# Kernel optimization log

Hardware: AMD Instinct MI355X
Metric: run time of the kernel (lower is better)

The kernel has to match this reference:

```python
import jax, jax.numpy as jnp
import numpy as np

SIGMA = 0.5          # init kwarg sigma
PATCH = 5            # init kwarg patch_size
TILE = 32            # init kwarg patch_distance (tile side)
H_PARAM = (PATCH // 2) ** 0.5  # self.h = sqrt(patch_size//2)


def _nlm(tiles, sigma, p, Hp):
    # tiles: [b, c, h, w] -- faithful jax port of nlm()
    b, c, h, w = tiles.shape
    pad = p // 2
    padded = jnp.pad(tiles, ((0, 0), (0, 0), (pad, pad), (pad, pad)), mode='edge')  # replicate pad
    # unfold: all p*p shifted views -> [b, c, p*p, h, w] (channel-major then patch index,
    # matching torch unfold + unflatten(1, (c, p*p)))
    pats = jnp.stack([padded[:, :, i:i + h, j:j + w]
                      for i in range(p) for j in range(p)], axis=2)
    center = p * p // 2
    keep = np.array([k for k in range(p * p) if k != center])
    N = h * w
    d = c * (p * p - 1)
    yN = pats[:, :, keep].reshape(b, d, N).transpose(0, 2, 1)  # [b, N, d]
    # pairwise euclidean distance (cdist)
    sq = jnp.sum(yN * yN, axis=-1)  # [b, N]
    d2 = sq[:, :, None] + sq[:, None, :] - 2.0 * jnp.einsum('bnd,bmd->bnm', yN, yN)
    dist = jnp.sqrt(jnp.maximum(d2, 0.0))  # [b, N, N]
    density = jnp.exp(-dist / (2.0 * Hp ** 2 * sigma ** 2))
    # diag set to +inf in dist -> density diag = 0
    density = density * (1.0 - jnp.eye(N, dtype=density.dtype))
    weight = density / jnp.sum(density, axis=-1, keepdims=True)  # [b, N, N]
    y = tiles.reshape(b, c, N)  # [b, c, N]
    mmse = jnp.einsum('bnm,bcm->bcn', weight, y)  # weighted sum of pixel values
    return mmse.reshape(b, c, h, w)


def reference(image):
    # Tile image into non-overlapping TILE x TILE tiles, run nlm batched, fold back.
    b, c, h, w = image.shape
    T = TILE
    nh, nw = h // T, w // T
    tiles = image.reshape(b, c, nh, T, nw, T).transpose(0, 2, 4, 1, 3, 5)
    tiles = tiles.reshape(b * nh * nw, c, T, T)
    out = _nlm(tiles, SIGMA, PATCH, H_PARAM)
    out = out.reshape(b, nh, nw, c, T, T).transpose(0, 3, 1, 4, 2, 5)
    return out.reshape(b, c, h, w)


def setup_inputs() -> dict:
    key = jax.random.key(0)
    image = jax.random.uniform(key, (1, 3, 320, 320), dtype=jnp.float32)
    return {"image": image}
```

## Files before the change

kernel.cpp:

```cpp
#include <hip/hip_runtime.h>
#include <math.h>

#define TS   32
#define PT   36
#define NPIX 1024
#define DF   72
#define KP   96
#define IMH  320
#define IMW  320
#define NTW  10
#define NTILE 100

#define F_UNITS_PER_TILE 12288
#define FHI_BYTES (NTILE * F_UNITS_PER_TILE * 16)
#define SQ_OFF    (2 * FHI_BYTES)

#define K2LOG2E 2.0813689810056077f

typedef __attribute__((ext_vector_type(8))) short bf16x8;
typedef __attribute__((ext_vector_type(8))) unsigned short u16x8;
typedef __attribute__((ext_vector_type(4))) float f32x4;

__global__ __launch_bounds__(256)
void nlm_feat_kernel(const float* __restrict__ img,
                     u16x8* __restrict__ Fhi, float* __restrict__ Sq)
{
    __shared__ float Ploc[3][6][36];
    __shared__ int   ofsl[KP];
    const int tid  = threadIdx.x;
    const int part = blockIdx.x;
    const int tile = blockIdx.y;
    const int by   = (tile / NTW) * TS;
    const int bx   = (tile % NTW) * TS;
    const float* Pf = &Ploc[0][0][0];

    for (int idx = tid; idx < 3 * 6 * 36; idx += 256) {
        int c   = idx / 216;
        int rem = idx - c * 216;
        int yl  = rem / 36;
        int x   = rem - yl * 36;
        int y   = 2 * part + yl;
        int iy  = min(max(y - 2, 0), TS - 1);
        int ix  = min(max(x - 2, 0), TS - 1);
        Ploc[c][yl][x] = img[(c * IMH + by + iy) * IMW + bx + ix];
    }
    if (tid < KP) {
        int k = tid, v = 0;
        if (k < DF) {
            int c = k / 24, o = k - c * 24;
            int kk = o + (o >= 12);
            int i = kk / 5, j = kk - (kk / 5) * 5;
            v = c * 216 + i * 36 + j;
        }
        ofsl[k] = v;
    }
    __syncthreads();

    if (tid < 64) {
        int m  = part * 64 + tid;
        int my = m >> 5, mx = m & 31;
        int ly0 = my - 2 * part;
        float s = 0.f;
        #pragma unroll
        for (int k = 0; k < 25; ++k) {
            if (k == 12) continue;
            int i = k / 5, j = k - (k / 5) * 5;
            float v0 = Ploc[0][ly0 + i][mx + j];
            float v1 = Ploc[1][ly0 + i][mx + j];
            float v2 = Ploc[2][ly0 + i][mx + j];
            s = fmaf(v0, v0, s); s = fmaf(v1, v1, s); s = fmaf(v2, v2, s);
        }
        Sq[tile * NPIX + m] = s;
    }

    #pragma unroll
    for (int q = 0; q < 3; ++q) {
        int u    = part * 768 + q * 256 + tid;
        int row  = u & 15;
        int c4   = (u >> 4) & 3;
        int rks  = u >> 6;
        int ks   = rks - (rks / 3) * 3;
        int rt   = rks / 3;
        int r    = rt * 16 + row;
        int lbase = ((r >> 5) - 2 * part) * 36 + (r & 31);
        u16x8 h;
        #pragma unroll
        for (int j = 0; j < 8; ++j) {
            int k = ks * 32 + c4 * 8 + j;
            unsigned short hs = 0;
            if (k < DF) {
                float f = Pf[lbase + ofsl[k]];
                unsigned int uu = __float_as_uint(f);
                hs = (unsigned short)((uu + 0x7fffu + ((uu >> 16) & 1u)) >> 16);
            }
            h[j] = hs;
        }
        Fhi[tile * F_UNITS_PER_TILE + u] = h;
    }
}

__global__ __launch_bounds__(256)
__attribute__((amdgpu_waves_per_eu(2, 3)))
void nlm_gemm_kernel(const float* __restrict__ img,
                     const bf16x8* __restrict__ Fhi,
                     const float* __restrict__ Sq, float* __restrict__ out)
{
    __shared__ float red[4][32][4];
    const int tid  = threadIdx.x;
    const int lane = tid & 63;
    const int wv   = tid >> 6;
    const int tile = blockIdx.y;
    const int by   = (tile / NTW) * TS;
    const int bx   = (tile % NTW) * TS;
    const int rtA  = blockIdx.x * 2;
    const int quad = lane >> 4;
    const int col  = lane & 15;

    const bf16x8* FHt = Fhi + tile * F_UNITS_PER_TILE;
    const float*  Sqt = Sq + tile * NPIX;

    bf16x8 aH[2][3];
    #pragma unroll
    for (int t = 0; t < 2; ++t)
        #pragma unroll
        for (int ks = 0; ks < 3; ++ks)
            aH[t][ks] = FHt[((rtA + t) * 3 + ks) * 64 + lane];
    asm volatile(""
        : "+v"(aH[0][0]), "+v"(aH[0][1]), "+v"(aH[0][2]),
          "+v"(aH[1][0]), "+v"(aH[1][1]), "+v"(aH[1][2]));

    float sqnK[2][4];
    #pragma unroll
    for (int t = 0; t < 2; ++t)
        #pragma unroll
        for (int i = 0; i < 4; ++i)
            sqnK[t][i] = Sqt[(rtA + t) * 16 + quad * 4 + i] * K2LOG2E;

    float rowsum[2][4] = {};
    float oacc[2][4][3] = {};

    #pragma unroll 2
    for (int it = 0; it < 16; ++it) {
        const int mt = wv * 16 + it;
        bf16x8 bH[3];
        #pragma unroll
        for (int ks = 0; ks < 3; ++ks)
            bH[ks] = FHt[(mt * 3 + ks) * 64 + lane];
        const int m  = mt * 16 + col;
        float smK = Sqt[m] * K2LOG2E;
        int my = m >> 5, mx = m & 31;
        float y0 = img[(0 * IMH + by + my) * IMW + bx + mx];
        float y1 = img[(1 * IMH + by + my) * IMW + bx + mx];
        float y2 = img[(2 * IMH + by + my) * IMW + bx + mx];

        f32x4 C0 = {0.f, 0.f, 0.f, 0.f};
        f32x4 C1 = {0.f, 0.f, 0.f, 0.f};
        #pragma unroll
        for (int ks = 0; ks < 3; ++ks) {
            C0 = __builtin_amdgcn_mfma_f32_16x16x32_bf16(aH[0][ks], bH[ks], C0, 0, 0, 0);
            C1 = __builtin_amdgcn_mfma_f32_16x16x32_bf16(aH[1][ks], bH[ks], C1, 0, 0, 0);
        }
        #pragma unroll
        for (int t = 0; t < 2; ++t) {
            f32x4 C = t ? C1 : C0;
            int nb = (rtA + t) * 16 + quad * 4;
            #pragma unroll
            for (int i = 0; i < 4; ++i) {
                float s2   = fmaxf(fmaf(-2.0f * K2LOG2E, C[i], sqnK[t][i] + smK), 0.f);
                float dens = __builtin_amdgcn_exp2f(-__builtin_amdgcn_sqrtf(s2));
                if (m == nb + i) dens = 0.f;
                rowsum[t][i] += dens;
                oacc[t][i][0] = fmaf(dens, y0, oacc[t][i][0]);
                oacc[t][i][1] = fmaf(dens, y1, oacc[t][i][1]);
                oacc[t][i][2] = fmaf(dens, y2, oacc[t][i][2]);
            }
        }
    }

    #pragma unroll
    for (int mask = 1; mask < 16; mask <<= 1)
        #pragma unroll
        for (int t = 0; t < 2; ++t)
            #pragma unroll
            for (int i = 0; i < 4; ++i) {
                rowsum[t][i]  += __shfl_xor(rowsum[t][i],  mask, 64);
                oacc[t][i][0] += __shfl_xor(oacc[t][i][0], mask, 64);
                oacc[t][i][1] += __shfl_xor(oacc[t][i][1], mask, 64);
                oacc[t][i][2] += __shfl_xor(oacc[t][i][2], mask, 64);
            }

    if (col == 0) {
        #pragma unroll
        for (int t = 0; t < 2; ++t)
            #pragma unroll
            for (int i = 0; i < 4; ++i) {
                int lr = t * 16 + quad * 4 + i;
                red[wv][lr][0] = rowsum[t][i];
                red[wv][lr][1] = oacc[t][i][0];
                red[wv][lr][2] = oacc[t][i][1];
                red[wv][lr][3] = oacc[t][i][2];
            }
    }
    __syncthreads();

    if (tid < 32) {
        float s = 0.f, o0 = 0.f, o1 = 0.f, o2 = 0.f;
        #pragma unroll
        for (int w = 0; w < 4; ++w) {
            s  += red[w][tid][0];
            o0 += red[w][tid][1];
            o1 += red[w][tid][2];
            o2 += red[w][tid][3];
        }
        int n = rtA * 16 + tid;
        float inv = 1.f / s;
        int gy = by + (n >> 5), gx = bx + (n & 31);
        out[(0 * IMH + gy) * IMW + gx] = o0 * inv;
        out[(1 * IMH + gy) * IMW + gx] = o1 * inv;
        out[(2 * IMH + gy) * IMW + gx] = o2 * inv;
    }
}

extern "C" void kernel_launch(void* const* d_in, const int* in_sizes, int n_in,
                              void* d_out, int out_size, void* d_ws, size_t ws_size,
                              hipStream_t stream) {
    const float* img = (const float*)d_in[0];
    float* out = (float*)d_out;
    char* ws = (char*)d_ws;
    u16x8* Fhi = (u16x8*)ws;
    float* Sq  = (float*)(ws + SQ_OFF);

    dim3 fgrid(16, NTILE);
    nlm_feat_kernel<<<fgrid, 256, 0, stream>>>(img, Fhi, Sq);
    dim3 grid(32, NTILE);
    nlm_gemm_kernel<<<grid, 256, 0, stream>>>(img, (const bf16x8*)Fhi, Sq, out);
}
```

Baseline: 113.8 us.

## Compute weighted pixel sums and row sums with fp16 MFMA instead of VALU FMAs

The second product (density times pixel values, plus the row sum via a constant-one channel) now runs on 16x16x16 fp16 MFMA instead of per-lane FMAs followed by cross-lane shuffle reductions. Pixel values are staged in LDS as hi/lo fp16 pairs to keep precision, and the density is packed to fp16 with round-toward-zero conversion. The operand roles are swapped so the density tile lands directly in the A-operand layout, and the K2LOG2E scaling of the squared norms moves into the feature kernel. This removes the many FMAs and shuffle reductions per element but adds LDS staging, a barrier, and fp16 rounding error on the weights.

```diff
diff --git a/kernel.cpp b/kernel.cpp
--- a/kernel.cpp
+++ b/kernel.cpp
@@ -20,6 +20,8 @@
 typedef __attribute__((ext_vector_type(8))) short bf16x8;
 typedef __attribute__((ext_vector_type(8))) unsigned short u16x8;
 typedef __attribute__((ext_vector_type(4))) float f32x4;
+typedef __attribute__((ext_vector_type(4))) __fp16 f16x4;
+typedef __attribute__((ext_vector_type(2))) __fp16 f16x2;
 
 __global__ __launch_bounds__(256)
 void nlm_feat_kernel(const float* __restrict__ img,
@@ -70,7 +72,7 @@
             float v2 = Ploc[2][ly0 + i][mx + j];
             s = fmaf(v0, v0, s); s = fmaf(v1, v1, s); s = fmaf(v2, v2, s);
         }
-        Sq[tile * NPIX + m] = s;
+        Sq[tile * NPIX + m] = s * K2LOG2E;
     }
 
     #pragma unroll
@@ -103,9 +105,12 @@
 __attribute__((amdgpu_waves_per_eu(2, 3)))
 void nlm_gemm_kernel(const float* __restrict__ img,
                      const bf16x8* __restrict__ Fhi,
-                     const float* __restrict__ Sq, float* __restrict__ out)
+                     const float* __restrict__ SqK, float* __restrict__ out)
 {
-    __shared__ float red[4][32][4];
+    __shared__ __fp16 Yhi[4][1032];
+    __shared__ __fp16 Ylo[4][1032];
+    __shared__ float red[4][2][16][4];
+
     const int tid  = threadIdx.x;
     const int lane = tid & 63;
     const int wv   = tid >> 6;
@@ -115,109 +120,107 @@
     const int rtA  = blockIdx.x * 2;
     const int quad = lane >> 4;
     const int col  = lane & 15;
+    const int ycol = col & 3;
 
     const bf16x8* FHt = Fhi + tile * F_UNITS_PER_TILE;
-    const float*  Sqt = Sq + tile * NPIX;
-
-    bf16x8 aH[2][3];
+    const float*  Sqt = SqK + tile * NPIX;
+
+    for (int idx = tid; idx < 4096; idx += 256) {
+        int c = idx >> 10, m = idx & 1023;
+        float v = 1.0f;
+        if (c < 3) v = img[(c * IMH + by + (m >> 5)) * IMW + bx + (m & 31)];
+        __fp16 h = (__fp16)v;
+        Yhi[c][m] = h;
+        Ylo[c][m] = (__fp16)(v - (float)h);
+    }
+
+    bf16x8 bN[2][3];
     #pragma unroll
     for (int t = 0; t < 2; ++t)
         #pragma unroll
         for (int ks = 0; ks < 3; ++ks)
-            aH[t][ks] = FHt[((rtA + t) * 3 + ks) * 64 + lane];
+            bN[t][ks] = FHt[((rtA + t) * 3 + ks) * 64 + lane];
     asm volatile(""
-        : "+v"(aH[0][0]), "+v"(aH[0][1]), "+v"(aH[0][2]),
-          "+v"(aH[1][0]), "+v"(aH[1][1]), "+v"(aH[1][2]));
-
-    float sqnK[2][4];
+        : "+v"(bN[0][0]), "+v"(bN[0][1]), "+v"(bN[0][2]),
+          "+v"(bN[1][0]), "+v"(bN[1][1]), "+v"(bN[1][2]));
+
+    float snK[2];
     #pragma unroll
     for (int t = 0; t < 2; ++t)
-        #pragma unroll
-        for (int i = 0; i < 4; ++i)
-            sqnK[t][i] = Sqt[(rtA + t) * 16 + quad * 4 + i] * K2LOG2E;
-
-    float rowsum[2][4] = {};
-    float oacc[2][4][3] = {};
+        snK[t] = Sqt[(rtA + t) * 16 + col];
+
+    f32x4 Dpv0 = {0.f, 0.f, 0.f, 0.f};
+    f32x4 Dpv1 = {0.f, 0.f, 0.f, 0.f};
+
+    __syncthreads();
 
     #pragma unroll 2
     for (int it = 0; it < 16; ++it) {
         const int mt = wv * 16 + it;
-        bf16x8 bH[3];
+        bf16x8 aF[3];
         #pragma unroll
         for (int ks = 0; ks < 3; ++ks)
-            bH[ks] = FHt[(mt * 3 + ks) * 64 + lane];
-        const int m  = mt * 16 + col;
-        float smK = Sqt[m] * K2LOG2E;
-        int my = m >> 5, mx = m & 31;
-        float y0 = img[(0 * IMH + by + my) * IMW + bx + mx];
-        float y1 = img[(1 * IMH + by + my) * IMW + bx + mx];
-        float y2 = img[(2 * IMH + by + my) * IMW + bx + mx];
+            aF[ks] = FHt[(mt * 3 + ks) * 64 + lane];
+        const f32x4 sqm = *(const f32x4*)&Sqt[mt * 16 + quad * 4];
+        const int yb = mt * 16 + quad * 4;
+        const f16x4 bhi = *(const f16x4*)&Yhi[ycol][yb];
+        const f16x4 blo = *(const f16x4*)&Ylo[ycol][yb];
 
         f32x4 C0 = {0.f, 0.f, 0.f, 0.f};
         f32x4 C1 = {0.f, 0.f, 0.f, 0.f};
         #pragma unroll
         for (int ks = 0; ks < 3; ++ks) {
-            C0 = __builtin_amdgcn_mfma_f32_16x16x32_bf16(aH[0][ks], bH[ks], C0, 0, 0, 0);
-            C1 = __builtin_amdgcn_mfma_f32_16x16x32_bf16(aH[1][ks], bH[ks], C1, 0, 0, 0);
-        }
+            C0 = __builtin_amdgcn_mfma_f32_16x16x32_bf16(aF[ks], bN[0][ks], C0, 0, 0, 0);
+            C1 = __builtin_amdgcn_mfma_f32_16x16x32_bf16(aF[ks], bN[1][ks], C1, 0, 0, 0);
+        }
+
         #pragma unroll
         for (int t = 0; t < 2; ++t) {
             f32x4 C = t ? C1 : C0;
-            int nb = (rtA + t) * 16 + quad * 4;
+            float d[4];
             #pragma unroll
             for (int i = 0; i < 4; ++i) {
-                float s2   = fmaxf(fmaf(-2.0f * K2LOG2E, C[i], sqnK[t][i] + smK), 0.f);
-                float dens = __builtin_amdgcn_exp2f(-__builtin_amdgcn_sqrtf(s2));
-                if (m == nb + i) dens = 0.f;
-                rowsum[t][i] += dens;
-                oacc[t][i][0] = fmaf(dens, y0, oacc[t][i][0]);
-                oacc[t][i][1] = fmaf(dens, y1, oacc[t][i][1]);
-                oacc[t][i][2] = fmaf(dens, y2, oacc[t][i][2]);
-            }
-        }
-    }
-
-    #pragma unroll
-    for (int mask = 1; mask < 16; mask <<= 1)
-        #pragma unroll
-        for (int t = 0; t < 2; ++t)
-            #pragma unroll
-            for (int i = 0; i < 4; ++i) {
-                rowsum[t][i]  += __shfl_xor(rowsum[t][i],  mask, 64);
-                oacc[t][i][0] += __shfl_xor(oacc[t][i][0], mask, 64);
-                oacc[t][i][1] += __shfl_xor(oacc[t][i][1], mask, 64);
-                oacc[t][i][2] += __shfl_xor(oacc[t][i][2], mask, 64);
-            }
-
-    if (col == 0) {
-        #pragma unroll
-        for (int t = 0; t < 2; ++t)
-            #pragma unroll
-            for (int i = 0; i < 4; ++i) {
-                int lr = t * 16 + quad * 4 + i;
-                red[wv][lr][0] = rowsum[t][i];
-                red[wv][lr][1] = oacc[t][i][0];
-                red[wv][lr][2] = oacc[t][i][1];
-                red[wv][lr][3] = oacc[t][i][2];
-            }
+                float s2 = fmaxf(fmaf(-2.0f * K2LOG2E, C[i], sqm[i] + snK[t]), 0.f);
+                d[i] = __builtin_amdgcn_exp2f(-__builtin_amdgcn_sqrtf(s2));
+            }
+            if (mt == rtA + t) {
+                #pragma unroll
+                for (int i = 0; i < 4; ++i)
+                    if (quad * 4 + i == col) d[i] = 0.f;
+            }
+            f16x2 p0 = __builtin_amdgcn_cvt_pkrtz(d[0], d[1]);
+            f16x2 p1 = __builtin_amdgcn_cvt_pkrtz(d[2], d[3]);
+            f16x4 wp = __builtin_shufflevector(p0, p1, 0, 1, 2, 3);
+            if (t == 0) {
+                Dpv0 = __builtin_amdgcn_mfma_f32_16x16x16f16(wp, bhi, Dpv0, 0, 0, 0);
+                Dpv0 = __builtin_amdgcn_mfma_f32_16x16x16f16(wp, blo, Dpv0, 0, 0, 0);
+            } else {
+                Dpv1 = __builtin_amdgcn_mfma_f32_16x16x16f16(wp, bhi, Dpv1, 0, 0, 0);
+                Dpv1 = __builtin_amdgcn_mfma_f32_16x16x16f16(wp, blo, Dpv1, 0, 0, 0);
+            }
+        }
+    }
+
+    if (col < 4) {
+        #pragma unroll
+        for (int i = 0; i < 4; ++i) {
+            red[wv][0][quad * 4 + i][col] = Dpv0[i];
+            red[wv][1][quad * 4 + i][col] = Dpv1[i];
+        }
     }
     __syncthreads();
 
-    if (tid < 32) {
-        float s = 0.f, o0 = 0.f, o1 = 0.f, o2 = 0.f;
-        #pragma unroll
-        for (int w = 0; w < 4; ++w) {
-            s  += red[w][tid][0];
-            o0 += red[w][tid][1];
-            o1 += red[w][tid][2];
-            o2 += red[w][tid][3];
-        }
-        int n = rtA * 16 + tid;
-        float inv = 1.f / s;
-        int gy = by + (n >> 5), gx = bx + (n & 31);
-        out[(0 * IMH + gy) * IMW + gx] = o0 * inv;
-        out[(1 * IMH + gy) * IMW + gx] = o1 * inv;
-        out[(2 * IMH + gy) * IMW + gx] = o2 * inv;
+    if (tid < 128) {
+        int n = tid >> 2, c = tid & 3;
+        int t = n >> 4, r = n & 15;
+        float s = red[0][t][r][c] + red[1][t][r][c]
+                + red[2][t][r][c] + red[3][t][r][c];
+        float rs = __shfl(s, (tid & 63) | 3, 64);
+        if (c < 3) {
+            int nn = rtA * 16 + n;
+            int gy = by + (nn >> 5), gx = bx + (nn & 31);
+            out[(c * IMH + gy) * IMW + gx] = s * (1.0f / rs);
+        }
     }
 }
 
```

Result: slower. 129.4 us (+13.7%).
